# Optimization experiments

Measured on AMD Instinct MI355X. Metric: run time of the kernel, lower is better.

Reference implementation:

```python
import jax, jax.numpy as jnp
import numpy as np

VOCAB = 50000; D = 512; H = 512; HD = H // 2; L = 2
T = 2048; NTAGS = 20; START = 18; END = 19
NEG = -10000.0


def setup_inputs() -> dict:
    key = jax.random.key(0)
    ks = jax.random.split(key, 24)
    s = 0.05
    rn = lambda k, shape: jax.random.normal(k, shape, jnp.float32) * s
    inp = {}
    inp["sentence"] = jax.random.randint(ks[0], (T,), 0, VOCAB)
    inp["emb"] = rn(ks[1], (VOCAB, D))
    i = 2
    for l in range(L):
        din = D if l == 0 else H
        for d in ("f", "b"):
            inp[f"l{l}{d}_Wih"] = rn(ks[i], (4 * HD, din)); i += 1
            inp[f"l{l}{d}_Whh"] = rn(ks[i], (4 * HD, HD)); i += 1
            inp[f"l{l}{d}_bih"] = rn(ks[i], (4 * HD,)); i += 1
            inp[f"l{l}{d}_bhh"] = rn(ks[i], (4 * HD,)); i += 1
    inp["W_out"] = rn(ks[i], (NTAGS, H)); i += 1
    inp["b_out"] = rn(ks[i], (NTAGS,)); i += 1
    tr = jax.random.normal(ks[i], (NTAGS, NTAGS), jnp.float32)
    tr = tr.at[START, :].set(NEG).at[:, END].set(NEG)
    inp["transitions"] = tr
    return inp


def _lstm_dir(x, Wih, Whh, bih, bhh, reverse):
    # x: [T, din]; precompute input contribution to all 4 gates (i,f,g,o order).
    xg = x @ Wih.T + bih  # [T, 4*HD]
    h0 = jnp.zeros((Whh.shape[1],), x.dtype)

    def step(carry, xt):
        h, c = carry
        z = xt + h @ Whh.T + bhh
        i, f, g, o = jnp.split(z, 4)
        c = jax.nn.sigmoid(f) * c + jax.nn.sigmoid(i) * jnp.tanh(g)
        h = jax.nn.sigmoid(o) * jnp.tanh(c)
        return (h, c), h

    _, hs = jax.lax.scan(step, (h0, h0), xg, reverse=reverse)
    return hs  # [T, HD], outputs aligned with timesteps in both directions


def _feats(sentence, emb, layers, W_out, b_out):
    x = emb[sentence]  # [T, D]
    for (Wf, Uf, bf, cf, Wb, Ub, bb, cb) in layers:
        hf = _lstm_dir(x, Wf, Uf, bf, cf, False)
        hb = _lstm_dir(x, Wb, Ub, bb, cb, True)
        x = jnp.concatenate([hf, hb], axis=-1)  # [T, H]
    return x @ W_out.T + b_out  # [T, NTAGS]


def _viterbi(feats, transitions):
    v0 = jnp.full((NTAGS,), NEG, feats.dtype).at[START].set(0.0)

    def step(v, feat):
        scores = v[None, :] + transitions  # [next_tag, prev_tag]
        bp = jnp.argmax(scores, axis=1)
        v_new = jnp.max(scores, axis=1) + feat
        return v_new, bp

    v_last, bps = jax.lax.scan(step, v0, feats)  # bps: [T, NTAGS]
    terminal = v_last + transitions[END]
    best = jnp.argmax(terminal)
    score = terminal[best]

    def back(tag, bp):
        return bp[tag], tag  # emit tag at this timestep, move to its predecessor

    _, path = jax.lax.scan(back, best, bps, reverse=True)
    return score, path


def reference(sentence, emb, l0f_Wih, l0f_Whh, l0f_bih, l0f_bhh, l0b_Wih, l0b_Whh, l0b_bih, l0b_bhh, l1f_Wih, l1f_Whh, l1f_bih, l1f_bhh, l1b_Wih, l1b_Whh, l1b_bih, l1b_bhh, W_out, b_out, transitions):
    layers = [
        (l0f_Wih, l0f_Whh, l0f_bih, l0f_bhh, l0b_Wih, l0b_Whh, l0b_bih, l0b_bhh),
        (l1f_Wih, l1f_Whh, l1f_bih, l1f_bhh, l1b_Wih, l1b_Whh, l1b_bih, l1b_bhh),
    ]
    feats = _feats(sentence, emb, layers, W_out, b_out)
    return _viterbi(feats, transitions)
```

## Files before the change

### kernel.cpp

```cpp
#include <hip/hip_runtime.h>
#include <math.h>


#define T_LEN 2048
#define DMODEL 512
#define HD 256
#define NTAGS 20
#define START_TAG 18
#define END_TAG 19
#define NCAND 128

__device__ __forceinline__ float fsig(float x) {
  return 1.0f / (1.0f + __expf(-x));
}
__device__ __forceinline__ float ftanh(float x) {
  float xc = fminf(15.0f, fmaxf(-15.0f, x));
  float e = __expf(2.0f * xc);
  return (e - 1.0f) / (e + 1.0f);
}

__device__ __forceinline__ unsigned long long rd_l2(unsigned long long* p) {
  unsigned long long old;
  unsigned long long zero = 0;
  asm volatile("global_atomic_add_x2 %0, %1, %2, off sc0\n\ts_waitcnt vmcnt(0)"
               : "=&v"(old)
               : "v"(p), "v"(zero)
               : "memory");
  return old;
}
__device__ __forceinline__ void pub_l2(unsigned long long* p,
                                       unsigned long long v) {
  *(volatile unsigned long long*)p = v;
}

__global__ void embed_k(const int* __restrict__ sent,
                        const float* __restrict__ emb,
                        float* __restrict__ x0) {
  int t = blockIdx.x;
  int tid = threadIdx.x;
  int tok = sent[t];
  const float4* src = (const float4*)(emb + (size_t)tok * DMODEL);
  float4* dst = (float4*)(x0 + (size_t)t * DMODEL);
  dst[tid] = src[tid];
}

__global__ __launch_bounds__(256) void gemm_xg_k(
    const float* __restrict__ X,
    const float* __restrict__ Wf, const float* __restrict__ Wb,
    const float* __restrict__ bf, const float* __restrict__ bb,
    float* __restrict__ outf, float* __restrict__ outb) {
  int bx = blockIdx.x;
  int by = blockIdx.y;
  int dir = blockIdx.z;
  const float* W = dir ? Wb : Wf;
  const float* bias = dir ? bb : bf;
  float* out = dir ? outb : outf;

  __shared__ __align__(16) float Xs[16][132];
  __shared__ __align__(16) float Ws[16][132];

  int tid = threadIdx.x;
  int tx = tid & 15;
  int ty = tid >> 4;

  float acc[8][8];
#pragma unroll
  for (int i = 0; i < 8; i++)
#pragma unroll
    for (int j = 0; j < 8; j++) acc[i][j] = 0.0f;

  for (int kt = 0; kt < DMODEL / 16; kt++) {
    __syncthreads();
#pragma unroll
    for (int l = 0; l < 2; l++) {
      int fi = tid + l * 256;
      int row = fi >> 2;
      int kq = fi & 3;
      float4 xv = *(const float4*)(X + (size_t)(by * 128 + row) * DMODEL + kt * 16 + kq * 4);
      Xs[kq * 4 + 0][row] = xv.x;
      Xs[kq * 4 + 1][row] = xv.y;
      Xs[kq * 4 + 2][row] = xv.z;
      Xs[kq * 4 + 3][row] = xv.w;
      float4 wv = *(const float4*)(W + (size_t)(bx * 128 + row) * DMODEL + kt * 16 + kq * 4);
      Ws[kq * 4 + 0][row] = wv.x;
      Ws[kq * 4 + 1][row] = wv.y;
      Ws[kq * 4 + 2][row] = wv.z;
      Ws[kq * 4 + 3][row] = wv.w;
    }
    __syncthreads();
#pragma unroll
    for (int k = 0; k < 16; k++) {
      float4 a0 = *(const float4*)&Xs[k][ty * 4];
      float4 a1 = *(const float4*)&Xs[k][64 + ty * 4];
      float4 b0 = *(const float4*)&Ws[k][tx * 4];
      float4 b1 = *(const float4*)&Ws[k][64 + tx * 4];
      float a[8] = {a0.x, a0.y, a0.z, a0.w, a1.x, a1.y, a1.z, a1.w};
      float b[8] = {b0.x, b0.y, b0.z, b0.w, b1.x, b1.y, b1.z, b1.w};
#pragma unroll
      for (int i = 0; i < 8; i++)
#pragma unroll
        for (int j = 0; j < 8; j++) acc[i][j] += a[i] * b[j];
    }
  }

  float4 bv0 = *(const float4*)(bias + bx * 128 + tx * 4);
  float4 bv1 = *(const float4*)(bias + bx * 128 + 64 + tx * 4);
  float bb8[8] = {bv0.x, bv0.y, bv0.z, bv0.w, bv1.x, bv1.y, bv1.z, bv1.w};
#pragma unroll
  for (int i = 0; i < 8; i++) {
    int row = by * 128 + ((i < 4) ? (ty * 4 + i) : (64 + ty * 4 + (i - 4)));
    float4 o0 = {acc[i][0] + bb8[0], acc[i][1] + bb8[1], acc[i][2] + bb8[2], acc[i][3] + bb8[3]};
    float4 o1 = {acc[i][4] + bb8[4], acc[i][5] + bb8[5], acc[i][6] + bb8[6], acc[i][7] + bb8[7]};
    *(float4*)(out + (size_t)row * 1024 + bx * 128 + tx * 4) = o0;
    *(float4*)(out + (size_t)row * 1024 + bx * 128 + 64 + tx * 4) = o1;
  }
}

__global__ __launch_bounds__(256, 1) void recur_k(
    const float* __restrict__ xg_f, const float* __restrict__ xg_b,
    const float* __restrict__ Whh_f, const float* __restrict__ Whh_b,
    const float* __restrict__ bhh_f, const float* __restrict__ bhh_b,
    float* __restrict__ xnext, unsigned long long* __restrict__ hcomm_base,
    int* __restrict__ elect_base, unsigned long long* __restrict__ probe_base,
    int* __restrict__ vote_base) {
  int dir = blockIdx.y;
  int tid = threadIdx.x;

  int xcd;
  asm volatile("s_getreg_b32 %0, hwreg(HW_REG_XCC_ID)" : "=s"(xcd));
  xcd &= 7;
  int* cnt = elect_base + dir * (1 + NCAND);
  int* tab = cnt + 1;

  __shared__ int e_tab[NCAND];
  __shared__ int e_info[4];
  __shared__ int probe_ok[8];
  if (tid == 0) {
    int ticket = __hip_atomic_fetch_add(cnt, 1, __ATOMIC_RELAXED,
                                        __HIP_MEMORY_SCOPE_AGENT);
    __hip_atomic_store(&tab[ticket], xcd + 1, __ATOMIC_RELAXED,
                       __HIP_MEMORY_SCOPE_AGENT);
    e_info[0] = ticket;
  }
  if (tid < NCAND) {
    int v;
    do {
      v = __hip_atomic_load(&tab[tid], __ATOMIC_RELAXED,
                            __HIP_MEMORY_SCOPE_AGENT);
    } while (v == 0);
    e_tab[tid] = v - 1;
  }
  __syncthreads();
  if (tid == 0) {
    int ticket = e_info[0];
    int counts[8] = {0, 0, 0, 0, 0, 0, 0, 0};
    int home = -1;
    for (int i = 0; i < NCAND; i++) {
      int x = e_tab[i];
      counts[x]++;
      if (counts[x] == 8 && home < 0) home = x;
    }
    int sel = 0, kc = 0, probe = 0;
    if (home >= 0) {
      if (xcd == home) {
        int rank = 0;
        for (int i = 0; i < ticket; i++)
          if (e_tab[i] == home) rank++;
        if (rank < 8) { sel = 1; kc = rank; probe = 1; }
      }
    } else {
      if (ticket < 8) { sel = 1; kc = ticket; probe = 0; }
    }
    e_info[1] = sel; e_info[2] = kc; e_info[3] = probe;
  }
  __syncthreads();
  if (!e_info[1]) return;
  int kc = e_info[2];
  int do_probe = e_info[3];
  int use_l2 = 0;

  if (do_probe) {
    unsigned long long* probe = probe_base + (size_t)dir * 8 * 16;
    int* vote = vote_base + dir * 8;
    if (tid == 0) {
      pub_l2(&probe[kc * 16], 0xBEEF000000000000ull + (unsigned)kc);
    }
    if (tid < 8) {
      int found = 0;
      for (int iter = 0; iter < 3000 && !found; ++iter) {
        if (rd_l2(&probe[tid * 16]) ==
            0xBEEF000000000000ull + (unsigned)tid) found = 1;
      }
      probe_ok[tid] = found;
    }
    __syncthreads();
    if (tid == 0) {
      int ok = 1;
      for (int i = 0; i < 8; i++) ok &= probe_ok[i];
      __hip_atomic_store(&vote[kc], 1 + ok, __ATOMIC_RELAXED,
                         __HIP_MEMORY_SCOPE_AGENT);
    }
    if (tid < 8) {
      int v;
      do {
        v = __hip_atomic_load(&vote[tid], __ATOMIC_RELAXED,
                              __HIP_MEMORY_SCOPE_AGENT);
      } while (v == 0);
      probe_ok[tid] = v;
    }
    __syncthreads();
    if (tid == 0) {
      int all2 = 1;
      for (int i = 0; i < 8; i++) all2 &= (probe_ok[i] == 2);
      e_info[3] = all2;
    }
    __syncthreads();
    use_l2 = e_info[3];
  }

  const float* Whh = dir ? Whh_b : Whh_f;
  const float* bhh = dir ? bhh_b : bhh_f;
  const float* xg = dir ? xg_b : xg_f;
  unsigned long long* hcomm = hcomm_base + (size_t)dir * 2 * HD;

  int r = tid >> 1;
  int half = tid & 1;
  int g = r >> 5;
  int kl = r & 31;
  int grow = g * 256 + kc * 32 + kl;

  float4 Wv[32];
  const float4* wrow = (const float4*)(Whh + (size_t)grow * HD + half * 128);
#pragma unroll
  for (int j = 0; j < 32; j++) Wv[j] = wrow[j];
  float bias = bhh[grow];

  __shared__ __align__(16) float hbuf[HD];
  __shared__ float zbuf[128];
  hbuf[tid] = 0.0f;
  __syncthreads();

  float c = 0.0f;
  bool is_remote = ((tid >> 5) != kc);

#pragma unroll 1
  for (int it = 0; it < T_LEN; ++it) {
    int t = dir ? (T_LEN - 1 - it) : it;
    int p = it & 1;
    unsigned int tag = (unsigned)(it + 1);

    float xgv = 0.0f;
    if (!half) xgv = xg[(size_t)t * 1024 + grow];

    const float4* h4 = (const float4*)hbuf + half * 32;
    float4 acc = {0.f, 0.f, 0.f, 0.f};
#pragma unroll
    for (int j = 0; j < 32; j++) {
      float4 hv = h4[j];
      acc.x += Wv[j].x * hv.x;
      acc.y += Wv[j].y * hv.y;
      acc.z += Wv[j].z * hv.z;
      acc.w += Wv[j].w * hv.w;
    }
    float s = (acc.x + acc.y) + (acc.z + acc.w);
    s += __shfl_xor(s, 1, 64);
    if (!half) zbuf[r] = s + xgv + bias;
    __syncthreads();

    if (tid < 32) {
      float zi = zbuf[tid];
      float zf = zbuf[32 + tid];
      float zg = zbuf[64 + tid];
      float zo = zbuf[96 + tid];
      c = fsig(zf) * c + fsig(zi) * ftanh(zg);
      float h = fsig(zo) * ftanh(c);
      union { float f; unsigned u; } cv;
      cv.f = h;
      unsigned long long pkt = ((unsigned long long)tag << 32) | cv.u;
      if (use_l2) {
        pub_l2(&hcomm[p * HD + kc * 32 + tid], pkt);
      } else {
        __hip_atomic_store(&hcomm[p * HD + kc * 32 + tid], pkt,
                           __ATOMIC_RELAXED, __HIP_MEMORY_SCOPE_AGENT);
      }
      xnext[(size_t)t * DMODEL + dir * HD + kc * 32 + tid] = h;
      hbuf[kc * 32 + tid] = h;
    }
    if (is_remote) {
      unsigned long long v;
      if (use_l2) {
        do { v = rd_l2(&hcomm[p * HD + tid]); } while ((unsigned)(v >> 32) != tag);
      } else {
        do {
          v = __hip_atomic_load(&hcomm[p * HD + tid], __ATOMIC_RELAXED,
                                __HIP_MEMORY_SCOPE_AGENT);
        } while ((unsigned)(v >> 32) != tag);
      }
      union { unsigned u; float f; } cv;
      cv.u = (unsigned)v;
      hbuf[tid] = cv.f;
    }
    __syncthreads();
  }
}

__global__ void proj_k(const float* __restrict__ x2,
                       const float* __restrict__ Wo,
                       const float* __restrict__ bo,
                       float* __restrict__ feats) {
  int t = blockIdx.x;
  int tid = threadIdx.x;
  int n = tid & 31;
  int seg = tid >> 5;
  __shared__ float red[8][32];
  float s = 0.0f;
  if (n < NTAGS) {
    const float* xr = x2 + (size_t)t * DMODEL + seg * 64;
    const float* wr = Wo + (size_t)n * DMODEL + seg * 64;
#pragma unroll
    for (int j = 0; j < 64; j++) s += xr[j] * wr[j];
  }
  red[seg][n] = s;
  __syncthreads();
  if (tid < NTAGS) {
    float tot = bo[tid];
#pragma unroll
    for (int k = 0; k < 8; k++) tot += red[k][tid];
    feats[(size_t)t * NTAGS + tid] = tot;
  }
}

__global__ void viterbi_k(const float* __restrict__ feats,
                          const float* __restrict__ tr,
                          float* __restrict__ out) {
  __shared__ float v[NTAGS];
  __shared__ unsigned char bp[T_LEN * NTAGS];
  __shared__ float term[NTAGS];
  int tid = threadIdx.x;

  float trrow[NTAGS];
  if (tid < NTAGS) {
#pragma unroll
    for (int p = 0; p < NTAGS; p++) trrow[p] = tr[tid * NTAGS + p];
    v[tid] = (tid == START_TAG) ? 0.0f : -10000.0f;
  }
  __syncthreads();

#pragma unroll 1
  for (int t = 0; t < T_LEN; t++) {
    float fv = 0.0f;
    if (tid < NTAGS) fv = feats[(size_t)t * NTAGS + tid];
    float best = -3.4e38f;
    int arg = 0;
    if (tid < NTAGS) {
#pragma unroll
      for (int p = 0; p < NTAGS; p++) {
        float sc = v[p] + trrow[p];
        if (sc > best) { best = sc; arg = p; }
      }
      bp[t * NTAGS + tid] = (unsigned char)arg;
    }
    __syncthreads();
    if (tid < NTAGS) v[tid] = best + fv;
    __syncthreads();
  }

  if (tid < NTAGS) term[tid] = v[tid] + tr[END_TAG * NTAGS + tid];
  __syncthreads();
  if (tid == 0) {
    float bs = term[0];
    int bi = 0;
    for (int p = 1; p < NTAGS; p++) {
      if (term[p] > bs) { bs = term[p]; bi = p; }
    }
    out[0] = bs;
    int tag = bi;
    for (int t = T_LEN - 1; t >= 0; t--) {
      out[1 + t] = (float)tag;
      tag = bp[t * NTAGS + tag];
    }
  }
}

extern "C" void kernel_launch(void* const* d_in, const int* in_sizes, int n_in,
                              void* d_out, int out_size, void* d_ws, size_t ws_size,
                              hipStream_t stream) {
  const int* sent = (const int*)d_in[0];
  const float* emb = (const float*)d_in[1];
  const float* l0f_Wih = (const float*)d_in[2];
  const float* l0f_Whh = (const float*)d_in[3];
  const float* l0f_bih = (const float*)d_in[4];
  const float* l0f_bhh = (const float*)d_in[5];
  const float* l0b_Wih = (const float*)d_in[6];
  const float* l0b_Whh = (const float*)d_in[7];
  const float* l0b_bih = (const float*)d_in[8];
  const float* l0b_bhh = (const float*)d_in[9];
  const float* l1f_Wih = (const float*)d_in[10];
  const float* l1f_Whh = (const float*)d_in[11];
  const float* l1f_bih = (const float*)d_in[12];
  const float* l1f_bhh = (const float*)d_in[13];
  const float* l1b_Wih = (const float*)d_in[14];
  const float* l1b_Whh = (const float*)d_in[15];
  const float* l1b_bih = (const float*)d_in[16];
  const float* l1b_bhh = (const float*)d_in[17];
  const float* W_out = (const float*)d_in[18];
  const float* b_out = (const float*)d_in[19];
  const float* transitions = (const float*)d_in[20];

  char* ws = (char*)d_ws;
  size_t off = 0;
  float* x0 = (float*)(ws + off);  off += (size_t)T_LEN * DMODEL * 4;
  float* xgf = (float*)(ws + off); off += (size_t)T_LEN * 1024 * 4;
  float* xgb = (float*)(ws + off); off += (size_t)T_LEN * 1024 * 4;
  float* x1 = (float*)(ws + off);  off += (size_t)T_LEN * DMODEL * 4;
  float* x2 = (float*)(ws + off);  off += (size_t)T_LEN * DMODEL * 4;
  float* feats = (float*)(ws + off); off += (size_t)T_LEN * NTAGS * 4;

  off = (off + 127) & ~(size_t)127;
  char* sync_area = ws + off;
  unsigned long long* hcomm0 = (unsigned long long*)(sync_area);
  unsigned long long* hcomm1 = (unsigned long long*)(sync_area + 8192);
  int* elect0 = (int*)(sync_area + 16384);
  int* elect1 = (int*)(sync_area + 18432);
  unsigned long long* probe0 = (unsigned long long*)(sync_area + 20480);
  unsigned long long* probe1 = (unsigned long long*)(sync_area + 22528);
  int* vote0 = (int*)(sync_area + 24576);
  int* vote1 = (int*)(sync_area + 25600);
  size_t sync_bytes = 26624;
  off += sync_bytes;

  float* outf = (float*)d_out;

  (void)hipMemsetAsync(sync_area, 0, sync_bytes, stream);

  embed_k<<<dim3(T_LEN), dim3(128), 0, stream>>>(sent, emb, x0);

  gemm_xg_k<<<dim3(8, 16, 2), dim3(256), 0, stream>>>(
      x0, l0f_Wih, l0b_Wih, l0f_bih, l0b_bih, xgf, xgb);

  recur_k<<<dim3(NCAND, 2), dim3(256), 0, stream>>>(
      xgf, xgb, l0f_Whh, l0b_Whh, l0f_bhh, l0b_bhh, x1, hcomm0, elect0,
      probe0, vote0);

  gemm_xg_k<<<dim3(8, 16, 2), dim3(256), 0, stream>>>(
      x1, l1f_Wih, l1b_Wih, l1f_bih, l1b_bih, xgf, xgb);

  recur_k<<<dim3(NCAND, 2), dim3(256), 0, stream>>>(
      xgf, xgb, l1f_Whh, l1b_Whh, l1f_bhh, l1b_bhh, x2, hcomm1, elect1,
      probe1, vote1);

  proj_k<<<dim3(T_LEN), dim3(256), 0, stream>>>(x2, W_out, b_out, feats);

  viterbi_k<<<dim3(1), dim3(64), 0, stream>>>(feats, transitions, outf);
}
```

Measured before the change: 7.824 ms.

## Replicate hidden-state mailboxes per consumer block and prefetch next-step gate inputs

Each producer now writes its hidden-state packet to eight per-consumer mailbox copies, each padded to its own cache line, so consumers poll private lines instead of all contending on one shared line. The input-gate value for the next timestep is loaded one iteration ahead to hide its global-memory latency, and an empty asm barrier pins the recurrent weights in registers. The cost is eight times more publish stores per step and a much larger sync workspace.

```diff
diff --git a/kernel.cpp b/kernel.cpp
--- a/kernel.cpp
+++ b/kernel.cpp
@@ -9,6 +9,9 @@
 #define START_TAG 18
 #define END_TAG 19
 #define NCAND 128
+
+#define HSLOT(cons, p, entry) (((((size_t)(cons)) * 2 + (p)) * 256 + (entry)) * 8)
+#define HCOMM_U64_PER_DIR (8 * 2 * 256 * 8)
 
 __device__ __forceinline__ float fsig(float x) {
   return 1.0f / (1.0f + __expf(-x));
@@ -221,7 +224,7 @@
   const float* Whh = dir ? Whh_b : Whh_f;
   const float* bhh = dir ? bhh_b : bhh_f;
   const float* xg = dir ? xg_b : xg_f;
-  unsigned long long* hcomm = hcomm_base + (size_t)dir * 2 * HD;
+  unsigned long long* hcomm = hcomm_base + (size_t)dir * HCOMM_U64_PER_DIR;
 
   int r = tid >> 1;
   int half = tid & 1;
@@ -233,6 +236,11 @@
   const float4* wrow = (const float4*)(Whh + (size_t)grow * HD + half * 128);
 #pragma unroll
   for (int j = 0; j < 32; j++) Wv[j] = wrow[j];
+#pragma unroll
+  for (int j = 0; j < 32; j++) {
+    asm volatile("" : "+v"(Wv[j].x), "+v"(Wv[j].y), "+v"(Wv[j].z),
+                      "+v"(Wv[j].w));
+  }
   float bias = bhh[grow];
 
   __shared__ __align__(16) float hbuf[HD];
@@ -242,6 +250,12 @@
 
   float c = 0.0f;
   bool is_remote = ((tid >> 5) != kc);
+
+  float xgv_next = 0.0f;
+  {
+    int t0 = dir ? (T_LEN - 1) : 0;
+    if (!half) xgv_next = xg[(size_t)t0 * 1024 + grow];
+  }
 
 #pragma unroll 1
   for (int it = 0; it < T_LEN; ++it) {
@@ -249,8 +263,11 @@
     int p = it & 1;
     unsigned int tag = (unsigned)(it + 1);
 
-    float xgv = 0.0f;
-    if (!half) xgv = xg[(size_t)t * 1024 + grow];
+    float xgv = xgv_next;
+    if (it + 1 < T_LEN) {
+      int tn = dir ? (T_LEN - 2 - it) : (it + 1);
+      if (!half) xgv_next = xg[(size_t)tn * 1024 + grow];
+    }
 
     const float4* h4 = (const float4*)hbuf + half * 32;
     float4 acc = {0.f, 0.f, 0.f, 0.f};
@@ -277,22 +294,30 @@
       union { float f; unsigned u; } cv;
       cv.f = h;
       unsigned long long pkt = ((unsigned long long)tag << 32) | cv.u;
+      int entry = kc * 32 + tid;
       if (use_l2) {
-        pub_l2(&hcomm[p * HD + kc * 32 + tid], pkt);
+#pragma unroll
+        for (int j = 0; j < 8; j++) {
+          pub_l2(&hcomm[HSLOT(j, p, entry)], pkt);
+        }
       } else {
-        __hip_atomic_store(&hcomm[p * HD + kc * 32 + tid], pkt,
-                           __ATOMIC_RELAXED, __HIP_MEMORY_SCOPE_AGENT);
+#pragma unroll
+        for (int j = 0; j < 8; j++) {
+          __hip_atomic_store(&hcomm[HSLOT(j, p, entry)], pkt,
+                             __ATOMIC_RELAXED, __HIP_MEMORY_SCOPE_AGENT);
+        }
       }
-      xnext[(size_t)t * DMODEL + dir * HD + kc * 32 + tid] = h;
-      hbuf[kc * 32 + tid] = h;
+      xnext[(size_t)t * DMODEL + dir * HD + entry] = h;
+      hbuf[entry] = h;
     }
     if (is_remote) {
+      unsigned long long* myslot = &hcomm[HSLOT(kc, p, tid)];
       unsigned long long v;
       if (use_l2) {
-        do { v = rd_l2(&hcomm[p * HD + tid]); } while ((unsigned)(v >> 32) != tag);
+        do { v = rd_l2(myslot); } while ((unsigned)(v >> 32) != tag);
       } else {
         do {
-          v = __hip_atomic_load(&hcomm[p * HD + tid], __ATOMIC_RELAXED,
+          v = __hip_atomic_load(myslot, __ATOMIC_RELAXED,
                                 __HIP_MEMORY_SCOPE_AGENT);
         } while ((unsigned)(v >> 32) != tag);
       }
@@ -418,15 +443,17 @@
 
   off = (off + 127) & ~(size_t)127;
   char* sync_area = ws + off;
+  size_t hcomm_bytes = (size_t)2 * HCOMM_U64_PER_DIR * 8;
   unsigned long long* hcomm0 = (unsigned long long*)(sync_area);
-  unsigned long long* hcomm1 = (unsigned long long*)(sync_area + 8192);
-  int* elect0 = (int*)(sync_area + 16384);
-  int* elect1 = (int*)(sync_area + 18432);
-  unsigned long long* probe0 = (unsigned long long*)(sync_area + 20480);
-  unsigned long long* probe1 = (unsigned long long*)(sync_area + 22528);
-  int* vote0 = (int*)(sync_area + 24576);
-  int* vote1 = (int*)(sync_area + 25600);
-  size_t sync_bytes = 26624;
+  unsigned long long* hcomm1 = (unsigned long long*)(sync_area + hcomm_bytes);
+  char* aux = sync_area + 2 * hcomm_bytes;
+  int* elect0 = (int*)(aux);
+  int* elect1 = (int*)(aux + 2048);
+  unsigned long long* probe0 = (unsigned long long*)(aux + 4096);
+  unsigned long long* probe1 = (unsigned long long*)(aux + 6144);
+  int* vote0 = (int*)(aux + 8192);
+  int* vote1 = (int*)(aux + 9216);
+  size_t sync_bytes = 2 * hcomm_bytes + 10240;
   off += sync_bytes;
 
   float* outf = (float*)d_out;
```

Result: slower. 18.82 ms (+140.6%).
